# Kernel optimization log

Hardware: AMD Instinct MI355X
Metric: run time of the kernel (lower is better)

Reference implementation:

```python
import jax, jax.numpy as jnp
import numpy as np

HIDDEN = 2048
NUM_HEADS = 16
NUM_KV_HEADS = 4
HEAD_DIM = HIDDEN // NUM_HEADS  # 128
GROUP = NUM_HEADS // NUM_KV_HEADS  # 4
SCALE = HEAD_DIM ** -0.5


def setup_inputs() -> dict:
    key = jax.random.key(0)
    ks = jax.random.split(key, 9)
    B, S = 2, 2048
    kv_dim = HEAD_DIM * NUM_KV_HEADS
    std = HIDDEN ** -0.5
    return {
        "x": jax.random.normal(ks[0], (B, S, HIDDEN), dtype=jnp.float32),
        "Wq": jax.random.normal(ks[1], (HIDDEN, HIDDEN), dtype=jnp.float32) * std,
        "bq": jnp.zeros((HIDDEN,), dtype=jnp.float32),
        "Wk": jax.random.normal(ks[2], (HIDDEN, kv_dim), dtype=jnp.float32) * std,
        "bk": jnp.zeros((kv_dim,), dtype=jnp.float32),
        "Wv": jax.random.normal(ks[3], (HIDDEN, kv_dim), dtype=jnp.float32) * std,
        "bv": jnp.zeros((kv_dim,), dtype=jnp.float32),
        "Wo": jax.random.normal(ks[4], (HIDDEN, HIDDEN), dtype=jnp.float32) * std,
        "bo": jnp.zeros((HIDDEN,), dtype=jnp.float32),
    }


def reference(x, Wq, bq, Wk, bk, Wv, bv, Wo, bo):
    B, S, _ = x.shape
    # projections
    q = (x @ Wq + bq).reshape(B, S, NUM_KV_HEADS, GROUP, HEAD_DIM)  # grouped query heads
    k = (x @ Wk + bk).reshape(B, S, NUM_KV_HEADS, HEAD_DIM)
    v = (x @ Wv + bv).reshape(B, S, NUM_KV_HEADS, HEAD_DIM)
    # scores: [B, Hkv, G, Sq, Sk] -- same math as repeat_interleave of K/V over G,
    # but K/V are broadcast over the group axis instead of materialized.
    attn = jnp.einsum("bqhgd,bkhd->bhgqk", q, k) * SCALE
    attn = jax.nn.softmax(attn, axis=-1)
    out = jnp.einsum("bhgqk,bkhd->bqhgd", attn, v).reshape(B, S, HIDDEN)
    return out @ Wo + bo
```

## Files before the change

kernel.cpp:

```cpp
#include <hip/hip_runtime.h>


#define SEQ    2048
#define HIDDEN 2048

typedef __attribute__((ext_vector_type(8))) short v8s;
typedef __attribute__((ext_vector_type(4))) float v4f;

#define MFMA16(a,b,c) __builtin_amdgcn_mfma_f32_16x16x32_bf16((a),(b),(c),0,0,0)

__device__ __forceinline__ ushort f2b(float f){
  unsigned u = __float_as_uint(f);
  u += 0x7fffu + ((u >> 16) & 1u);
  return (ushort)(u >> 16);
}

__device__ __forceinline__ unsigned cvt_pk_bf16(float lo, float hi){
  unsigned r;
  asm("v_cvt_pk_bf16_f32 %0, %1, %2" : "=v"(r) : "v"(lo), "v"(hi));
  return r;
}

__device__ __forceinline__ void gload16(const void* g, void* l){
  __builtin_amdgcn_global_load_lds((const __attribute__((address_space(1))) void*)g,
                                   (__attribute__((address_space(3))) void*)l, 16, 0, 0);
}

#define WAIT_VM0   0x0F70
#define WAIT_VM2   0x0F72
#define WAIT_LGKM0 0xC07F

__global__ void k_conv(const float* __restrict__ in, ushort* __restrict__ out, int n){
  int i = (blockIdx.x*256 + threadIdx.x)*4;
  if (i >= n) return;
  float4 f = *(const float4*)(in + i);
  ushort4 u; u.x=f2b(f.x); u.y=f2b(f.y); u.z=f2b(f.z); u.w=f2b(f.w);
  *(ushort4*)(out + i) = u;
}

__global__ void k_tconv(const float* __restrict__ in, ushort* __restrict__ out,
                        int rows, int cols){
  __shared__ float t[32][33];
  int tx = threadIdx.x & 31, ty = threadIdx.x >> 5;
  int c0 = blockIdx.x*32, r0 = blockIdx.y*32;
#pragma unroll
  for (int i=0;i<4;i++) t[ty+i*8][tx] = in[(size_t)(r0+ty+i*8)*cols + c0+tx];
  __syncthreads();
#pragma unroll
  for (int i=0;i<4;i++) out[(size_t)(c0+ty+i*8)*rows + r0+tx] = f2b(t[tx][ty+i*8]);
}

__global__ void k_tv(const ushort* __restrict__ vb, ushort* __restrict__ vT){
  __shared__ ushort t[32][33];
  int tx = threadIdx.x & 31, ty = threadIdx.x >> 5;
  int s0 = blockIdx.x*32, d0 = blockIdx.y*32, bh = blockIdx.z;
  int b = bh >> 2, h = bh & 3;
  const ushort* src = vb + (size_t)b*SEQ*512 + h*128;
#pragma unroll
  for (int i=0;i<4;i++) t[ty+i*8][tx] = src[(size_t)(s0+ty+i*8)*512 + d0+tx];
  __syncthreads();
  ushort* dst = vT + (size_t)bh*128*SEQ;
#pragma unroll
  for (int i=0;i<4;i++) dst[(size_t)(d0+ty+i*8)*SEQ + s0+tx] = t[tx][ty+i*8];
}

#define GEMM256_MAIN(A_, Bt_)                                                          \
  __shared__ ushort sA[2][2][128*64], sB[2][2][128*64];                                \
  const int tid = threadIdx.x, lane = tid & 63, w = tid >> 6;                          \
  const int wm = w >> 2, wn = w & 3, lm = lane & 15, quad = lane >> 4;                 \
  const int wh = wn >> 1, wl = wn & 1, l3 = lane >> 3, l7m = lm & 7;                   \
  const int swz = ((lane & 7) ^ (l3 & 7)) * 8;                                         \
  const int rowB = blockIdx.y*256, colB = blockIdx.x*256;                              \
  const ushort* Ag = (A_); const ushort* Bg = (Bt_);                                   \
  v4f acc[8][4] = {};                                                                  \
  STG_A(0,0,0) STG_A(0,1,0) STG_B(0,0,0) STG_B(0,1,0) STG_A(1,0,1)                     \
  __builtin_amdgcn_s_waitcnt(WAIT_VM2);                                                \
  __builtin_amdgcn_s_barrier(); __builtin_amdgcn_sched_barrier(0);                     \
  for (int t = 0; t < 32; t++){                                                        \
    const int p = t & 1, pn = p ^ 1;                                                   \
    const int tn  = (t+1 < 32) ? t+1 : t;                                              \
    const int tnn = (t+2 < 32) ? t+2 : 31;                                             \
    v8s a0[4][2], a1[4][2], bb0[2][2], bb1[2][2];                                      \
                                                                              \
    _Pragma("unroll")                                                                  \
    for (int i=0;i<4;i++){ LDA(a0[i][0], i, 0) LDA(a0[i][1], i, 1) }                   \
    _Pragma("unroll")                                                                  \
    for (int j=0;j<2;j++){ LDB(bb0[j][0], j, 0) LDB(bb0[j][1], j, 1) }                 \
    STG_A(tn, 1, pn)                                                                   \
    __builtin_amdgcn_s_barrier(); __builtin_amdgcn_sched_barrier(0);                   \
    __builtin_amdgcn_s_waitcnt(WAIT_LGKM0); __builtin_amdgcn_sched_barrier(0);         \
    __builtin_amdgcn_s_setprio(1);                                                     \
    _Pragma("unroll")                                                                  \
    for (int ks=0;ks<2;ks++)                                                           \
      _Pragma("unroll")                                                                \
      for (int i=0;i<4;i++)                                                            \
        _Pragma("unroll")                                                              \
        for (int j=0;j<2;j++) acc[i][j] = MFMA16(a0[i][ks], bb0[j][ks], acc[i][j]);    \
    __builtin_amdgcn_s_setprio(0);                                                     \
    __builtin_amdgcn_s_barrier(); __builtin_amdgcn_sched_barrier(0);                   \
                                                                              \
    _Pragma("unroll")                                                                  \
    for (int j=0;j<2;j++){ LDB(bb1[j][0], j+2, 0) LDB(bb1[j][1], j+2, 1) }             \
    STG_B(tn, 0, pn)                                                                   \
    __builtin_amdgcn_s_barrier(); __builtin_amdgcn_sched_barrier(0);                   \
    __builtin_amdgcn_s_waitcnt(WAIT_LGKM0); __builtin_amdgcn_sched_barrier(0);         \
    __builtin_amdgcn_s_setprio(1);                                                     \
    _Pragma("unroll")                                                                  \
    for (int ks=0;ks<2;ks++)                                                           \
      _Pragma("unroll")                                                                \
      for (int i=0;i<4;i++)                                                            \
        _Pragma("unroll")                                                              \
        for (int j=0;j<2;j++) acc[i][j+2] = MFMA16(a0[i][ks], bb1[j][ks], acc[i][j+2]);\
    __builtin_amdgcn_s_setprio(0);                                                     \
    __builtin_amdgcn_s_barrier(); __builtin_amdgcn_sched_barrier(0);                   \
                                                                              \
    _Pragma("unroll")                                                                  \
    for (int i=0;i<4;i++){ LDA(a1[i][0], i+4, 0) LDA(a1[i][1], i+4, 1) }               \
    STG_B(tn, 1, pn)                                                                   \
    __builtin_amdgcn_s_barrier(); __builtin_amdgcn_sched_barrier(0);                   \
    __builtin_amdgcn_s_waitcnt(WAIT_LGKM0); __builtin_amdgcn_sched_barrier(0);         \
    __builtin_amdgcn_s_setprio(1);                                                     \
    _Pragma("unroll")                                                                  \
    for (int ks=0;ks<2;ks++)                                                           \
      _Pragma("unroll")                                                                \
      for (int i=0;i<4;i++)                                                            \
        _Pragma("unroll")                                                              \
        for (int j=0;j<2;j++) acc[i+4][j] = MFMA16(a1[i][ks], bb0[j][ks], acc[i+4][j]);\
    __builtin_amdgcn_s_setprio(0);                                                     \
    __builtin_amdgcn_s_barrier(); __builtin_amdgcn_sched_barrier(0);                   \
                  \
    STG_A(tnn, 0, p)                                                                   \
    __builtin_amdgcn_s_waitcnt(WAIT_VM2); __builtin_amdgcn_sched_barrier(0);           \
    __builtin_amdgcn_s_barrier(); __builtin_amdgcn_sched_barrier(0);                   \
    __builtin_amdgcn_s_setprio(1);                                                     \
    _Pragma("unroll")                                                                  \
    for (int ks=0;ks<2;ks++)                                                           \
      _Pragma("unroll")                                                                \
      for (int i=0;i<4;i++)                                                            \
        _Pragma("unroll")                                                              \
        for (int j=0;j<2;j++)                                                          \
          acc[i+4][j+2] = MFMA16(a1[i][ks], bb1[j][ks], acc[i+4][j+2]);                \
    __builtin_amdgcn_s_setprio(0);                                                     \
    __builtin_amdgcn_s_barrier(); __builtin_amdgcn_sched_barrier(0);                   \
  }

#define STG_A(t_, h_, buf_) { _Pragma("unroll") for (int i_=0;i_<2;i_++){              \
    int c_ = w*2 + i_;                                                                 \
    gload16(Ag + (size_t)(rowB + (h_)*128 + c_*8 + l3)*HIDDEN + (t_)*64 + swz,         \
            &sA[buf_][h_][c_*512 + lane*8]); } }
#define STG_B(t_, h_, buf_) { _Pragma("unroll") for (int i_=0;i_<2;i_++){              \
    int c_ = w*2 + i_;                                                                 \
    gload16(Bg + (size_t)(colB + (h_)*128 + c_*8 + l3)*HIDDEN + (t_)*64 + swz,         \
            &sB[buf_][h_][c_*512 + lane*8]); } }
#define LDA(dst_, i_, ks_) dst_ = *(const v8s*)(&sA[p][wm][((i_)*16+lm)*64 + ((((ks_)*4+quad))^l7m)*8]);
#define LDB(dst_, j_, ks_) dst_ = *(const v8s*)(&sB[p][wh][(wl*64 + (j_)*16+lm)*64 + ((((ks_)*4+quad))^l7m)*8]);

__global__ __launch_bounds__(512, 1) void k_gemm_qkv(
    const ushort* __restrict__ A, const ushort* __restrict__ Bt,
    const float* __restrict__ bq, const float* __restrict__ bk, const float* __restrict__ bv,
    ushort* __restrict__ qb, ushort* __restrict__ kb, ushort* __restrict__ vb){
  GEMM256_MAIN(A, Bt)
#pragma unroll
  for (int i=0;i<8;i++)
#pragma unroll
  for (int j=0;j<4;j++){
    int col = colB + wn*64 + j*16 + lm;
#pragma unroll
    for (int r=0;r<4;r++){
      int row = rowB + wm*128 + i*16 + quad*4 + r;
      float v = acc[i][j][r];
      if (col < 2048)      qb[(size_t)row*2048 + col]        = f2b(v + bq[col]);
      else if (col < 2560) kb[(size_t)row*512 + (col-2048)]  = f2b(v + bk[col-2048]);
      else                 vb[(size_t)row*512 + (col-2560)]  = f2b(v + bv[col-2560]);
    }
  }
}

__global__ __launch_bounds__(512, 1) void k_gemm_out(
    const ushort* __restrict__ A, const ushort* __restrict__ Bt,
    const float* __restrict__ bo, float* __restrict__ out){
  GEMM256_MAIN(A, Bt)
#pragma unroll
  for (int i=0;i<8;i++)
#pragma unroll
  for (int j=0;j<4;j++){
    int col = colB + wn*64 + j*16 + lm;
#pragma unroll
    for (int r=0;r<4;r++){
      int row = rowB + wm*128 + i*16 + quad*4 + r;
      out[(size_t)row*2048 + col] = acc[i][j][r] + bo[col];
    }
  }
}

__global__ __launch_bounds__(512, 2) void k_attn(
    const ushort* __restrict__ qb, const ushort* __restrict__ kb,
    const ushort* __restrict__ vT, ushort* __restrict__ Ob){
  __shared__ ushort sK[2][64*128];
  __shared__ ushort sV[2][128*64];
  __shared__ ushort sP[8][1024];
  const int tid = threadIdx.x, lane = tid & 63, w = tid >> 6;
  const int lm = lane & 15, quad = lane >> 4, q8 = quad*8;
  const int pair = blockIdx.x & 7;
  const int hkv = pair & 3, b = pair >> 2;
  const int qt = (blockIdx.x >> 3) & 15, g = blockIdx.x >> 7;
  const int head = hkv*4 + g;
  const float C = 0.08838834764831845f * 1.4426950408889634f;

  const ushort* kbb = kb + (size_t)b*SEQ*512 + hkv*128;
  const ushort* vbb = vT + (size_t)(b*4+hkv)*128*SEQ;

  const int kk = lane >> 4, ksw = lane & 15;
  const int dd = lane >> 3, vsw = lane & 7;

#define STAGE_K(t, buf) { _Pragma("unroll") for (int i=0;i<2;i++){                     \
    int c = w*2 + i; int key = c*4 + kk; int wd = ksw ^ (key & 15);                    \
    gload16(kbb + (size_t)((t)*64 + key)*512 + wd*8, &sK[buf][c*512 + lane*8]); } }
#define STAGE_V(t, buf) { _Pragma("unroll") for (int i=0;i<2;i++){                     \
    int c = w*2 + i; int drow = c*8 + dd; int wd = vsw ^ dd;                           \
    gload16(vbb + (size_t)drow*SEQ + (t)*64 + wd*8, &sV[buf][c*512 + lane*8]); } }

  v8s qf[4];
#pragma unroll
  for (int ks=0; ks<4; ks++)
    qf[ks] = *(const v8s*)(qb + (size_t)(b*SEQ + qt*128 + w*16 + lm)*HIDDEN
                              + head*128 + ks*32 + q8);

  v4f o[8] = {};
  float lreg = 0.f;

  STAGE_K(0, 0)
  STAGE_V(0, 0)
  __builtin_amdgcn_s_waitcnt(WAIT_VM0);
  __syncthreads();

  for (int t=0; t<32; t++){
    const int cur = t & 1;
    if (t < 31) STAGE_K(t+1, cur^1)

    v4f sacc[4] = {};
#pragma unroll
    for (int ks=0; ks<4; ks++){
      v8s kf[4];
#pragma unroll
      for (int kt=0; kt<4; kt++)
        kf[kt] = *(const v8s*)(&sK[cur][(kt*16+lm)*128 + ((ks*4+quad)^lm)*8]);
      __builtin_amdgcn_s_setprio(1);
#pragma unroll
      for (int kt=0; kt<4; kt++)
        sacc[kt] = MFMA16(kf[kt], qf[ks], sacc[kt]);
      __builtin_amdgcn_s_setprio(0);
    }

    {
      float rs = 0.f;
#pragma unroll
      for (int kt=0; kt<4; kt++){
        float p0 = __builtin_amdgcn_exp2f(sacc[kt][0]*C);
        float p1 = __builtin_amdgcn_exp2f(sacc[kt][1]*C);
        float p2 = __builtin_amdgcn_exp2f(sacc[kt][2]*C);
        float p3 = __builtin_amdgcn_exp2f(sacc[kt][3]*C);
        rs += (p0+p1)+(p2+p3);
        uint2 pk;
        pk.x = cvt_pk_bf16(p0, p1);
        pk.y = cvt_pk_bf16(p2, p3);
        int kc = kt >> 1;
        int dl = ((kt&1)*2 + (quad>>1))*16 + lm;
        *(uint2*)(&sP[w][kc*512 + dl*8 + (quad&1)*4]) = pk;
      }
      lreg += rs;
    }

    __builtin_amdgcn_s_waitcnt(WAIT_VM0);
    __syncthreads();
    if (t < 31) STAGE_V(t+1, cur^1)

    __builtin_amdgcn_s_waitcnt(WAIT_LGKM0);
    v8s pa[2];
#pragma unroll
    for (int kc=0; kc<2; kc++)
      pa[kc] = *(const v8s*)(&sP[w][kc*512 + lane*8]);
#pragma unroll
    for (int kc=0; kc<2; kc++){
      v8s vf[8];
#pragma unroll
      for (int dt=0; dt<8; dt++)
        vf[dt] = *(const v8s*)(&sV[cur][(dt*16+lm)*64 + ((kc*4+quad)^(lm&7))*8]);
      __builtin_amdgcn_s_setprio(1);
#pragma unroll
      for (int dt=0; dt<8; dt++)
        o[dt] = MFMA16(pa[kc], vf[dt], o[dt]);
      __builtin_amdgcn_s_setprio(0);
    }
  }

  {
    float lv = lreg;
    lv += __shfl_xor(lv, 16);
    lv += __shfl_xor(lv, 32);
    float inv[4];
#pragma unroll
    for (int r=0;r<4;r++) inv[r] = 1.0f / __shfl(lv, (lane & 48) + quad*4 + r);
#pragma unroll
    for (int dt=0; dt<8; dt++)
#pragma unroll
      for (int r=0;r<4;r++){
        int row = b*SEQ + qt*128 + w*16 + quad*4 + r;
        int col = head*128 + dt*16 + lm;
        Ob[(size_t)row*HIDDEN + col] = f2b(o[dt][r]*inv[r]);
      }
  }
#undef STAGE_K
#undef STAGE_V
}

extern "C" void kernel_launch(void* const* d_in, const int* in_sizes, int n_in,
                              void* d_out, int out_size, void* d_ws, size_t ws_size,
                              hipStream_t stream){
  const float* x  = (const float*)d_in[0];
  const float* Wq = (const float*)d_in[1];
  const float* bq = (const float*)d_in[2];
  const float* Wk = (const float*)d_in[3];
  const float* bk = (const float*)d_in[4];
  const float* Wv = (const float*)d_in[5];
  const float* bv = (const float*)d_in[6];
  const float* Wo = (const float*)d_in[7];
  const float* bo = (const float*)d_in[8];
  float* out = (float*)d_out;

  ushort* xb  = (ushort*)d_ws;
  ushort* Wt  = xb  + 8388608;
  ushort* Wto = Wt  + 6291456;
  ushort* qb  = Wto + 4194304;
  ushort* kb  = qb  + 8388608;
  ushort* vb  = kb  + 2097152;
  ushort* vT  = vb  + 2097152;
  ushort* Ob  = vT  + 2097152;

  k_conv <<<8192, 256, 0, stream>>>(x, xb, 8388608);
  k_tconv<<<dim3(64,64), 256, 0, stream>>>(Wq, Wt, 2048, 2048);
  k_tconv<<<dim3(16,64), 256, 0, stream>>>(Wk, Wt + 4194304, 2048, 512);
  k_tconv<<<dim3(16,64), 256, 0, stream>>>(Wv, Wt + 5242880, 2048, 512);
  k_tconv<<<dim3(64,64), 256, 0, stream>>>(Wo, Wto, 2048, 2048);
  k_gemm_qkv<<<dim3(12,16), 512, 0, stream>>>(xb, Wt, bq, bk, bv, qb, kb, vb);
  k_tv  <<<dim3(64,4,8), 256, 0, stream>>>(vb, vT);
  k_attn<<<512, 512, 0, stream>>>(qb, kb, vT, Ob);
  k_gemm_out<<<dim3(8,16), 512, 0, stream>>>(Ob, Wto, bo, out);
}
```

Before: 348.2 us.

## Remap GEMM blocks across XCDs and shrink output GEMM tile to 128x256

Both GEMMs now use a 1D grid whose block index is remapped so that blocks dispatched round-robin to the same XCD (flat & 7) get neighbouring tiles, with the intent of improving L2 reuse of A and B panels. The output projection GEMM also switches from 256x256 to 128x256 tiles, raising its block count from 128 to 256 so the CUs are better filled. The smaller tile halves the A-side reuse per block and adds more B reloads from memory. The remapping assumes the GPU has 8 XCDs.

```diff
diff --git a/kernel.cpp b/kernel.cpp
--- a/kernel.cpp
+++ b/kernel.cpp
@@ -70,7 +70,6 @@
   const int wm = w >> 2, wn = w & 3, lm = lane & 15, quad = lane >> 4;                 \
   const int wh = wn >> 1, wl = wn & 1, l3 = lane >> 3, l7m = lm & 7;                   \
   const int swz = ((lane & 7) ^ (l3 & 7)) * 8;                                         \
-  const int rowB = blockIdx.y*256, colB = blockIdx.x*256;                              \
   const ushort* Ag = (A_); const ushort* Bg = (Bt_);                                   \
   v4f acc[8][4] = {};                                                                  \
   STG_A(0,0,0) STG_A(0,1,0) STG_B(0,0,0) STG_B(0,1,0) STG_A(1,0,1)                     \
@@ -159,6 +158,10 @@
     const ushort* __restrict__ A, const ushort* __restrict__ Bt,
     const float* __restrict__ bq, const float* __restrict__ bk, const float* __restrict__ bv,
     ushort* __restrict__ qb, ushort* __restrict__ kb, ushort* __restrict__ vb){
+  const int flat = blockIdx.x;
+  const int nf = (flat & 7) * 24 + (flat >> 3);
+  const int rowB = (nf & 15) * 256;
+  const int colB = (nf >> 4) * 256;
   GEMM256_MAIN(A, Bt)
 #pragma unroll
   for (int i=0;i<8;i++)
@@ -179,18 +182,84 @@
 __global__ __launch_bounds__(512, 1) void k_gemm_out(
     const ushort* __restrict__ A, const ushort* __restrict__ Bt,
     const float* __restrict__ bo, float* __restrict__ out){
-  GEMM256_MAIN(A, Bt)
-#pragma unroll
-  for (int i=0;i<8;i++)
+  __shared__ ushort sA[2][128*64], sB[2][2][128*64];
+  const int tid = threadIdx.x, lane = tid & 63, w = tid >> 6;
+  const int wm = w >> 2, wn = w & 3, lm = lane & 15, quad = lane >> 4;
+  const int wh = wn >> 1, wl = wn & 1, l3 = lane >> 3, l7m = lm & 7;
+  const int swz = ((lane & 7) ^ (l3 & 7)) * 8;
+  const int flat = blockIdx.x;
+  const int nf = (flat & 7) * 32 + (flat >> 3);
+  const int rowB = (nf & 31) * 128;
+  const int colB = (nf >> 5) * 256;
+  const ushort* Ag = A; const ushort* Bg = Bt;
+  v4f acc[4][4] = {};
+
+#define OSTG_A(t_, buf_) { _Pragma("unroll") for (int i_=0;i_<2;i_++){                 \
+    int c_ = w*2 + i_;                                                                 \
+    gload16(Ag + (size_t)(rowB + c_*8 + l3)*HIDDEN + (t_)*64 + swz,                    \
+            &sA[buf_][c_*512 + lane*8]); } }
+#define OSTG_B(t_, h_, buf_) { _Pragma("unroll") for (int i_=0;i_<2;i_++){             \
+    int c_ = w*2 + i_;                                                                 \
+    gload16(Bg + (size_t)(colB + (h_)*128 + c_*8 + l3)*HIDDEN + (t_)*64 + swz,         \
+            &sB[buf_][h_][c_*512 + lane*8]); } }
+#define OLDA(dst_, i_, ks_) dst_ = *(const v8s*)(&sA[p][(wm*64 + (i_)*16 + lm)*64 + ((((ks_)*4+quad))^l7m)*8]);
+#define OLDB(dst_, j_, ks_) dst_ = *(const v8s*)(&sB[p][wh][(wl*64 + (j_)*16 + lm)*64 + ((((ks_)*4+quad))^l7m)*8]);
+
+  OSTG_A(0,0) OSTG_B(0,0,0) OSTG_B(0,1,0) OSTG_A(1,1)
+  __builtin_amdgcn_s_waitcnt(WAIT_VM2);
+  __builtin_amdgcn_s_barrier(); __builtin_amdgcn_sched_barrier(0);
+  for (int t = 0; t < 32; t++){
+    const int p = t & 1, pn = p ^ 1;
+    const int tn  = (t+1 < 32) ? t+1 : t;
+    const int tnn = (t+2 < 32) ? t+2 : 31;
+    v8s a[4][2], b0[2][2], b1[2][2];
+#pragma unroll
+    for (int i=0;i<4;i++){ OLDA(a[i][0], i, 0) OLDA(a[i][1], i, 1) }
+#pragma unroll
+    for (int j=0;j<2;j++){ OLDB(b0[j][0], j, 0) OLDB(b0[j][1], j, 1) }
+    OSTG_B(tn, 0, pn)
+    __builtin_amdgcn_s_barrier(); __builtin_amdgcn_sched_barrier(0);
+    __builtin_amdgcn_s_waitcnt(WAIT_LGKM0); __builtin_amdgcn_sched_barrier(0);
+    __builtin_amdgcn_s_setprio(1);
+#pragma unroll
+    for (int ks=0;ks<2;ks++)
+#pragma unroll
+      for (int i=0;i<4;i++)
+#pragma unroll
+        for (int j=0;j<2;j++) acc[i][j] = MFMA16(a[i][ks], b0[j][ks], acc[i][j]);
+    __builtin_amdgcn_s_setprio(0);
+    __builtin_amdgcn_s_barrier(); __builtin_amdgcn_sched_barrier(0);
+#pragma unroll
+    for (int j=0;j<2;j++){ OLDB(b1[j][0], j+2, 0) OLDB(b1[j][1], j+2, 1) }
+    OSTG_B(tn, 1, pn) OSTG_A(tnn, p)
+    __builtin_amdgcn_s_waitcnt(WAIT_VM2); __builtin_amdgcn_sched_barrier(0);
+    __builtin_amdgcn_s_barrier(); __builtin_amdgcn_sched_barrier(0);
+    __builtin_amdgcn_s_waitcnt(WAIT_LGKM0); __builtin_amdgcn_sched_barrier(0);
+    __builtin_amdgcn_s_setprio(1);
+#pragma unroll
+    for (int ks=0;ks<2;ks++)
+#pragma unroll
+      for (int i=0;i<4;i++)
+#pragma unroll
+        for (int j=0;j<2;j++) acc[i][j+2] = MFMA16(a[i][ks], b1[j][ks], acc[i][j+2]);
+    __builtin_amdgcn_s_setprio(0);
+    __builtin_amdgcn_s_barrier(); __builtin_amdgcn_sched_barrier(0);
+  }
+#pragma unroll
+  for (int i=0;i<4;i++)
 #pragma unroll
   for (int j=0;j<4;j++){
     int col = colB + wn*64 + j*16 + lm;
 #pragma unroll
     for (int r=0;r<4;r++){
-      int row = rowB + wm*128 + i*16 + quad*4 + r;
+      int row = rowB + wm*64 + i*16 + quad*4 + r;
       out[(size_t)row*2048 + col] = acc[i][j][r] + bo[col];
     }
   }
+#undef OSTG_A
+#undef OSTG_B
+#undef OLDA
+#undef OLDB
 }
 
 __global__ __launch_bounds__(512, 2) void k_attn(
@@ -342,8 +411,8 @@
   k_tconv<<<dim3(16,64), 256, 0, stream>>>(Wk, Wt + 4194304, 2048, 512);
   k_tconv<<<dim3(16,64), 256, 0, stream>>>(Wv, Wt + 5242880, 2048, 512);
   k_tconv<<<dim3(64,64), 256, 0, stream>>>(Wo, Wto, 2048, 2048);
-  k_gemm_qkv<<<dim3(12,16), 512, 0, stream>>>(xb, Wt, bq, bk, bv, qb, kb, vb);
+  k_gemm_qkv<<<192, 512, 0, stream>>>(xb, Wt, bq, bk, bv, qb, kb, vb);
   k_tv  <<<dim3(64,4,8), 256, 0, stream>>>(vb, vT);
   k_attn<<<512, 512, 0, stream>>>(qb, kb, vT, Ob);
-  k_gemm_out<<<dim3(8,16), 512, 0, stream>>>(Ob, Wto, bo, out);
-}
+  k_gemm_out<<<256, 512, 0, stream>>>(Ob, Wto, bo, out);
+}
```

After: 346.7 us. About the same (-0.4%).
